# Kernel optimization log

Hardware: AMD Instinct MI355X
Metric: run time of the kernel (lower is better)

The kernel has to match this reference:

```python
import jax, jax.numpy as jnp
import numpy as np

EMBED = 256
HEADS = 8
HEAD_DIM = EMBED // HEADS  # 32, even for RoPE
INIT_VAL = 1.0
HEADS_RANGE = 3.0


def rotate_every_two(x):
    # (x1, x2) -> (-x2, x1) on interleaved pairs of last dim
    x1 = x[..., ::2]
    x2 = x[..., 1::2]
    return jnp.stack([-x2, x1], axis=-1).reshape(x.shape)


def theta_shift(x, sin, cos):
    # x: [B, heads, H, W, D]; sin/cos: [H, W, D] broadcast over B, heads
    return x * cos + rotate_every_two(x) * sin


def rel_pos_2d(H, W):
    # RetNetRelPos2d: RoPE angles + per-head exponential decay mask
    angle = 1.0 / (10000.0 ** jnp.linspace(0.0, 1.0, HEAD_DIM // 2))
    angle = jnp.repeat(angle, 2)  # [D]
    idx = jnp.arange(H * W, dtype=jnp.float32)
    sin = jnp.sin(idx[:, None] * angle[None, :]).reshape(H, W, HEAD_DIM)
    cos = jnp.cos(idx[:, None] * angle[None, :]).reshape(H, W, HEAD_DIM)
    h_idx = jnp.arange(HEADS, dtype=jnp.float32)
    decay = jnp.log(1.0 - 2.0 ** (-INIT_VAL - HEADS_RANGE * h_idx / HEADS))  # [heads]
    gh, gw = jnp.meshgrid(jnp.arange(H), jnp.arange(W), indexing='ij')
    grid = jnp.stack([gh, gw], axis=-1).reshape(H * W, 2)  # [N,2]
    dist = jnp.abs(grid[:, None, :] - grid[None, :, :]).sum(-1)  # [N,N] L1 distance
    mask = dist[None, :, :].astype(jnp.float32) * decay[:, None, None]  # [heads,N,N]
    return sin, cos, mask


def setup_inputs() -> dict:
    key = jax.random.key(0)
    ks = jax.random.split(key, 8)
    B, H, W, C = 2, 48, 48, EMBED
    s = 0.02
    return {
        'x': jax.random.normal(ks[0], (B, H, W, C), jnp.float32),
        'Wq': jax.random.normal(ks[1], (C, C), jnp.float32) * s,
        'bq': jnp.zeros((C,), jnp.float32),
        'Wk': jax.random.normal(ks[2], (C, C), jnp.float32) * s,
        'bk': jnp.zeros((C,), jnp.float32),
        'Wv': jax.random.normal(ks[3], (C, C), jnp.float32) * s,
        'bv': jnp.zeros((C,), jnp.float32),
        'lepe_w': jax.random.normal(ks[4], (C, 1, 5, 5), jnp.float32) * s,  # depthwise 5x5
        'lepe_b': jnp.zeros((C,), jnp.float32),
        'Wo': jax.random.normal(ks[5], (C, C), jnp.float32) * s,
        'bo': jnp.zeros((C,), jnp.float32),
    }


def reference(x, Wq, bq, Wk, bk, Wv, bv, lepe_w, lepe_b, Wo, bo):
    B, H, W, C = x.shape
    N = H * W
    sin, cos, mask = rel_pos_2d(H, W)
    scaling = HEAD_DIM ** -0.5

    q = x @ Wq + bq
    k = (x @ Wk + bk) * scaling
    v = x @ Wv + bv

    # lepe: depthwise 5x5 conv on v (BHWC)
    lepe = jax.lax.conv_general_dilated(
        v.transpose(0, 3, 1, 2), lepe_w, (1, 1), 'SAME',
        feature_group_count=C, dimension_numbers=('NCHW', 'OIHW', 'NCHW'))
    lepe = lepe.transpose(0, 2, 3, 1) + lepe_b  # [B,H,W,C]

    def split_heads(t):
        return t.reshape(B, H, W, HEADS, HEAD_DIM).transpose(0, 3, 1, 2, 4)

    qr = theta_shift(split_heads(q), sin, cos).reshape(B, HEADS, N, HEAD_DIM)
    kr = theta_shift(split_heads(k), sin, cos).reshape(B, HEADS, N, HEAD_DIM)
    vv = split_heads(v).reshape(B, HEADS, N, HEAD_DIM)

    attn = jnp.einsum('bhnd,bhmd->bhnm', qr, kr) + mask[None]  # [B,heads,N,N]
    attn = jax.nn.softmax(attn, axis=-1)
    out = jnp.einsum('bhnm,bhmd->bhnd', attn, vv)
    out = out.transpose(0, 2, 1, 3).reshape(B, H, W, C)
    out = out + lepe
    return out @ Wo + bo
```

## Files before the change

### kernel.cpp

```cpp
#include <hip/hip_runtime.h>
#include <hip/hip_bf16.h>
#include <math.h>

#define NN 2304
#define ROWSZ 4608
#define SZ (ROWSZ*256)

typedef __attribute__((ext_vector_type(8))) short short8;
typedef __attribute__((ext_vector_type(4))) float f32x4;

__device__ __forceinline__ float bf2f(unsigned short u) {
    return __uint_as_float(((unsigned int)u) << 16);
}
__device__ __forceinline__ unsigned short f2bf(float f) {
    unsigned int u = __float_as_uint(f);
    u += 0x7FFFu + ((u >> 16) & 1u);
    return (unsigned short)(u >> 16);
}
__device__ __forceinline__ unsigned int pack_bf2(float a, float b) {
    return (unsigned int)f2bf(a) | ((unsigned int)f2bf(b) << 16);
}

__device__ __forceinline__ float ub2f(unsigned int v, int r) {
#if defined(__has_builtin)
#if __has_builtin(__builtin_amdgcn_cvt_f32_ubyte0)
    switch (r) {
        case 0: return __builtin_amdgcn_cvt_f32_ubyte0(v);
        case 1: return __builtin_amdgcn_cvt_f32_ubyte1(v);
        case 2: return __builtin_amdgcn_cvt_f32_ubyte2(v);
        default: return __builtin_amdgcn_cvt_f32_ubyte3(v);
    }
#else
    return (float)((v >> (8*r)) & 0xFFu);
#endif
#else
    return (float)((v >> (8*r)) & 0xFFu);
#endif
}

__global__ __launch_bounds__(256) void prep_kernel(
    const void* __restrict__ x,
    const void* __restrict__ Wq, const void* __restrict__ bq,
    const void* __restrict__ Wk, const void* __restrict__ bk,
    const void* __restrict__ Wv, const void* __restrict__ bv,
    const void* __restrict__ Wo, const void* __restrict__ bo,
    const void* __restrict__ lw, const void* __restrict__ lb,
    int* __restrict__ flag, unsigned char* __restrict__ D,
    float2* __restrict__ scT, unsigned short* __restrict__ xb,
    unsigned short* __restrict__ Wt, float* __restrict__ bb,
    float* __restrict__ lwT)
{
    __shared__ float wsh[256][17];
    __shared__ int sflag;
    const int blk = blockIdx.x;
    const int t = threadIdx.x;

    {
        const int nq = blk;
        const int yq = (nq*21846) >> 20, xq = nq - yq*48;
        unsigned int* drow = reinterpret_cast<unsigned int*>(D + (size_t)nq*NN);
        for (int idx = t; idx < 576; idx += 256) {
            const int kp0 = idx*4;
            unsigned int wv = 0;
            #pragma unroll
            for (int r = 0; r < 4; ++r) {
                int kp = kp0 + r;
                int yk = (kp*21846) >> 20;
                int xk = kp - yk*48;
                unsigned int dist = __usad((unsigned)yq, (unsigned)yk,
                                    __usad((unsigned)xq, (unsigned)xk, 0u));
                wv |= dist << (8*r);
            }
            drow[idx] = wv;
        }
        if (t < 16) {
            const int j = t;
            const float ang = exp2f((float)j * (-0.8858474919699633f));
            float sv, cv;
            sincosf((float)nq * ang, &sv, &cv);
            scT[nq*16 + j] = make_float2(sv, cv);
        }
    }
    if (blk >= 656) return;

    {
        const unsigned int* xu = (const unsigned int*)x;
        if (t < 64) {
            int cnt = 0;
            for (int i = t; i < 256; i += 64) {
                unsigned int e = (xu[i] >> 7) & 0xFFu;
                cnt += (e < 87u || e > 167u) ? 1 : 0;
            }
            #pragma unroll
            for (int o = 32; o; o >>= 1) cnt += __shfl_down(cnt, o);
            if (t == 0) sflag = (cnt >= 32) ? 1 : 0;
        }
        __syncthreads();
    }
    const int F = sflag;
    if (blk == 0 && t == 0) *flag = F;

    if (blk < 576) {
        const int e = (blk*256 + t) * 8;
        if (F) {
            const float* xp = (const float*)x + e;
            float4 a0 = *reinterpret_cast<const float4*>(xp);
            float4 a1 = *reinterpret_cast<const float4*>(xp + 4);
            uint4 o;
            o.x = pack_bf2(a0.x, a0.y); o.y = pack_bf2(a0.z, a0.w);
            o.z = pack_bf2(a1.x, a1.y); o.w = pack_bf2(a1.z, a1.w);
            *reinterpret_cast<uint4*>(xb + e) = o;
        } else {
            *reinterpret_cast<uint4*>(xb + e) =
                *reinterpret_cast<const uint4*>((const unsigned short*)x + e);
        }
        return;
    }

    const int idx = blk - 576;
    const int m = idx >> 4;
    if (m == 4) {
        if ((idx & 15) != 0) return;
        float wv[25];
        #pragma unroll
        for (int j = 0; j < 25; ++j)
            wv[j] = F ? ((const float*)lw)[t*25 + j]
                      : bf2f(((const unsigned short*)lw)[t*25 + j]);
        #pragma unroll
        for (int j = 0; j < 25; ++j) lwT[j*256 + t] = wv[j];
        bb[4*256 + t] = F ? ((const float*)lb)[t]
                          : bf2f(((const unsigned short*)lb)[t]);
        return;
    }
    const int oc0 = (idx & 15) * 16;
    const void* W  = (m == 0) ? Wq : (m == 1) ? Wk : (m == 2) ? Wv : Wo;
    const void* bs = (m == 0) ? bq : (m == 1) ? bk : (m == 2) ? bv : bo;
    const float scale = (m == 1) ? 0.17677669529663687f * 1.4426950408889634f : 1.0f;
    #pragma unroll
    for (int j2 = 0; j2 < 16; ++j2)
        wsh[t][j2] = F ? ((const float*)W)[t*256 + oc0 + j2]
                       : bf2f(((const unsigned short*)W)[t*256 + oc0 + j2]);
    __syncthreads();
    const int j = t >> 4, seg = t & 15;
    unsigned int u[8];
    #pragma unroll
    for (int i = 0; i < 8; ++i) {
        float v0 = wsh[seg*16 + 2*i][j]     * scale;
        float v1 = wsh[seg*16 + 2*i + 1][j] * scale;
        u[i] = pack_bf2(v0, v1);
    }
    unsigned short* drow = Wt + ((size_t)(m*256 + oc0 + j))*256 + seg*16;
    *reinterpret_cast<uint4*>(drow)     = make_uint4(u[0], u[1], u[2], u[3]);
    *reinterpret_cast<uint4*>(drow + 8) = make_uint4(u[4], u[5], u[6], u[7]);
    if ((idx & 15) == 0)
        bb[m*256 + t] = (F ? ((const float*)bs)[t]
                           : bf2f(((const unsigned short*)bs)[t])) * scale;
}

__global__ __launch_bounds__(256) void qkv_mfma(
    const unsigned short* __restrict__ xb, const unsigned short* __restrict__ Wt,
    const float* __restrict__ bb, const float2* __restrict__ scT,
    unsigned short* __restrict__ q, unsigned short* __restrict__ k,
    unsigned short* __restrict__ v, unsigned short* __restrict__ vT)
{
    __shared__ __align__(16) char smem[43136];
    char* sc_lds = smem + 40960;
    const int t = threadIdx.x;
    const int w = t >> 6, lane = t & 63;
    const int q16 = lane & 15, quad = lane >> 4;
    const int m = blockIdx.y;
    const int tok0 = blockIdx.x * 16;
    const int b = (tok0 >= NN) ? 1 : 0;
    const int n0 = tok0 - b*NN;

    {
        float2 sv = scT[(size_t)(n0 + (t >> 4))*16 + (t & 15)];
        *reinterpret_cast<float2*>(sc_lds + (t >> 4)*136 + (t & 15)*8) = sv;
    }
    short8 af[8];
    #pragma unroll
    for (int kk = 0; kk < 8; ++kk)
        af[kk] = *reinterpret_cast<const short8*>(
            xb + (size_t)(tok0 + q16)*256 + kk*32 + quad*8);

    const unsigned short* Wm = Wt + (size_t)m*256*256;
    {
        const unsigned short* src = Wm + (size_t)t*256;
        #pragma unroll
        for (int s = 0; s < 4; ++s)
            *reinterpret_cast<uint4*>(smem + t*80 + s*16) =
                *reinterpret_cast<const uint4*>(src + s*8);
    }
    __syncthreads();

    f32x4 acc[4];
    #pragma unroll
    for (int tt = 0; tt < 4; ++tt) acc[tt] = (f32x4){0.f, 0.f, 0.f, 0.f};
    int cur = 0;
    for (int kk = 0; kk < 8; ++kk) {
        const int kkn = (kk < 7) ? kk + 1 : 7;
        uint4 nw[4];
        const unsigned short* src = Wm + (size_t)t*256 + kkn*32;
        #pragma unroll
        for (int s = 0; s < 4; ++s) nw[s] = *reinterpret_cast<const uint4*>(src + s*8);
        char* Wl = smem + cur*20480;
        #pragma unroll
        for (int tt = 0; tt < 4; ++tt) {
            short8 bf = *reinterpret_cast<const short8*>(
                Wl + (w*64 + tt*16 + q16)*80 + quad*16);
            acc[tt] = __builtin_amdgcn_mfma_f32_16x16x32_bf16(af[kk], bf, acc[tt], 0, 0, 0);
        }
        char* Wn = smem + (cur ^ 1)*20480;
        #pragma unroll
        for (int s = 0; s < 4; ++s)
            *reinterpret_cast<uint4*>(Wn + t*80 + s*16) = nw[s];
        __syncthreads();
        cur ^= 1;
    }

    char* ostage = smem;
    float bias[4];
    #pragma unroll
    for (int tt = 0; tt < 4; ++tt) bias[tt] = bb[m*256 + w*64 + tt*16 + q16];
    if (m < 2) {
        const int odd = q16 & 1;
        #pragma unroll
        for (int tt = 0; tt < 4; ++tt) {
            const int j = ((tt & 1) << 3) + (q16 >> 1);
            #pragma unroll
            for (int r = 0; r < 4; ++r) {
                const int tokL = quad*4 + r;
                float a = acc[tt][r] + bias[tt];
                float ap = __shfl_xor(a, 1);
                float2 sc = *reinterpret_cast<const float2*>(sc_lds + tokL*136 + j*8);
                float val = odd ? fmaf(a, sc.y, ap*sc.x) : fmaf(a, sc.y, -ap*sc.x);
                *reinterpret_cast<unsigned short*>(
                    ostage + tokL*528 + (w*64 + tt*16 + q16)*2) = f2bf(val);
            }
        }
    } else {
        #pragma unroll
        for (int tt = 0; tt < 4; ++tt) {
            #pragma unroll
            for (int r = 0; r < 4; ++r)
                *reinterpret_cast<unsigned short*>(
                    ostage + (quad*4 + r)*528 + (w*64 + tt*16 + q16)*2)
                    = f2bf(acc[tt][r] + bias[tt]);
        }
    }
    __syncthreads();
    unsigned short* dst = (m == 0) ? q : (m == 1) ? k : v;
    {
        char* p = ostage + (t >> 4)*528 + (t & 15)*32;
        uint4 a0 = *reinterpret_cast<uint4*>(p);
        uint4 a1 = *reinterpret_cast<uint4*>(p + 16);
        unsigned short* drow = dst + (size_t)(tok0 + (t >> 4))*256 + (t & 15)*16;
        *reinterpret_cast<uint4*>(drow)     = a0;
        *reinterpret_cast<uint4*>(drow + 8) = a1;
    }
    if (m == 2) {
        const int h = t >> 5, d = t & 31;
        unsigned int vp[8];
        #pragma unroll
        for (int i = 0; i < 8; ++i) {
            unsigned short e0 = *reinterpret_cast<unsigned short*>(
                ostage + (2*i)*528 + (h*32 + d)*2);
            unsigned short e1 = *reinterpret_cast<unsigned short*>(
                ostage + (2*i + 1)*528 + (h*32 + d)*2);
            vp[i] = (unsigned int)e0 | ((unsigned int)e1 << 16);
        }
        unsigned short* vt = vT + ((size_t)(b*8 + h)*32 + d)*NN + n0;
        *reinterpret_cast<uint4*>(vt)     = make_uint4(vp[0], vp[1], vp[2], vp[3]);
        *reinterpret_cast<uint4*>(vt + 8) = make_uint4(vp[4], vp[5], vp[6], vp[7]);
    }
}

__global__ __launch_bounds__(256) void lepe_kernel(const unsigned short* __restrict__ v,
    const float* __restrict__ lwT, const float* __restrict__ bb,
    unsigned short* __restrict__ lepe)
{
    int c = threadIdx.x;
    int pos = blockIdx.x;
    int b  = pos >= NN ? 1 : 0;
    int yx = pos - b*NN;
    int y  = (yx*21846) >> 20;
    int xx = yx - y*48;
    float acc = bb[4*256 + c];
    #pragma unroll
    for (int ky = 0; ky < 5; ++ky) {
        int yy = y + ky - 2;
        if ((unsigned)yy >= 48u) continue;
        #pragma unroll
        for (int kx = 0; kx < 5; ++kx) {
            int xc = xx + kx - 2;
            if ((unsigned)xc >= 48u) continue;
            acc = fmaf(bf2f(v[((b*NN + yy*48 + xc)<<8) + c]),
                       lwT[(ky*5 + kx)*256 + c], acc);
        }
    }
    lepe[(pos<<8) + c] = f2bf(acc);
}

template<int DIRECT>
__global__ __launch_bounds__(256) void attn_kernel(
    const unsigned short* __restrict__ q, const unsigned short* __restrict__ k,
    const unsigned short* __restrict__ vT, const unsigned char* __restrict__ D,
    unsigned short* __restrict__ o, float* __restrict__ pacc, float* __restrict__ pl)
{
    __shared__ char smem[27648];
    const int t = threadIdx.x;
    const int w = t >> 6, lane = t & 63;
    const int q16 = lane & 15, quad = lane >> 4;
    char* PsB = smem + 19456 + w*2048;
    const int bh = blockIdx.y, b = bh >> 3, h = bh & 7;
    const int q0 = blockIdx.x*64 + w*16;
    const int nq = q0 + q16;
    const float decay2 = log2f(1.0f - exp2f(-1.0f - 0.375f*(float)h));
    short8 qfrag = *reinterpret_cast<const short8*>(q + ((size_t)(b*NN + nq))*256 + h*32 + quad*8);
    f32x4 acc0 = {0.f,0.f,0.f,0.f}, acc1 = {0.f,0.f,0.f,0.f};
    const f32x4 zero = {0.f,0.f,0.f,0.f};
    float lacc = 0.0f;
    const unsigned short* kbase = k + (size_t)(b*NN)*256 + h*32;
    const unsigned short* vtb = vT + (size_t)bh*32*NN;
    const unsigned char* Dbase = D + (size_t)nq*NN + quad*4;
    const int skr = t >> 2, skp = t & 3;
    const int svd = t >> 3, svp = t & 7;
    const int psW = q16*16 + (quad & 1)*8;
    const int qsh = quad >> 1;
    const int nchunk = 36 / gridDim.z;
    const int kt0 = blockIdx.z * nchunk;

    {
        uint4 kraw = *reinterpret_cast<const uint4*>(kbase + (kt0*64 + skr)*256 + skp*8);
        uint4 vraw = *reinterpret_cast<const uint4*>(vtb + svd*NN + kt0*64 + svp*8);
        *reinterpret_cast<uint4*>(smem + skr*80 + skp*16) = kraw;
        *reinterpret_cast<uint4*>(smem + 5120 + svd*144 + svp*16) = vraw;
    }
    __syncthreads();

    int cur = 0;
    for (int kc = 0; kc < nchunk; ++kc) {
        const int kt = kt0 + kc;
        const int ktn = (kc + 1 < nchunk) ? kt + 1 : kt;
        uint4 nk = *reinterpret_cast<const uint4*>(kbase + (ktn*64 + skr)*256 + skp*8);
        uint4 nv = *reinterpret_cast<const uint4*>(vtb + svd*NN + ktn*64 + svp*8);
        unsigned int dw[4];
        #pragma unroll
        for (int tt = 0; tt < 4; ++tt)
            dw[tt] = *reinterpret_cast<const unsigned int*>(Dbase + kt*64 + tt*16);
        char* KsB = smem + cur*9728;
        char* VtB = KsB + 5120;
        f32x4 st[4];
        #pragma unroll
        for (int tt = 0; tt < 4; ++tt) {
            short8 kf = *reinterpret_cast<const short8*>(KsB + (tt*16 + q16)*80 + quad*16);
            st[tt] = __builtin_amdgcn_mfma_f32_16x16x32_bf16(kf, qfrag, zero, 0, 0, 0);
        }
        unsigned int pk[8];
        float lsum = 0.0f;
        #pragma unroll
        for (int tt = 0; tt < 4; ++tt) {
            float p[4];
            #pragma unroll
            for (int r = 0; r < 4; ++r) {
                p[r] = exp2f(fmaf(decay2, ub2f(dw[tt], r), st[tt][r]));
                lsum += p[r];
            }
            pk[tt*2]   = __builtin_amdgcn_perm(__float_as_uint(p[1]), __float_as_uint(p[0]), 0x07060302);
            pk[tt*2+1] = __builtin_amdgcn_perm(__float_as_uint(p[3]), __float_as_uint(p[2]), 0x07060302);
        }
        lacc += lsum;
        #pragma unroll
        for (int tt = 0; tt < 4; ++tt) {
            uint2 pp; pp.x = pk[tt*2]; pp.y = pk[tt*2+1];
            *reinterpret_cast<uint2*>(PsB + (tt >> 1)*1024 + (((tt*2) + qsh) & 3)*256 + psW) = pp;
        }
        #pragma unroll
        for (int kh = 0; kh < 2; ++kh) {
            short8 pf = *reinterpret_cast<const short8*>(PsB + kh*1024 + lane*16);
            short8 v0 = *reinterpret_cast<const short8*>(VtB + q16*144 + kh*64 + quad*16);
            short8 v1 = *reinterpret_cast<const short8*>(VtB + (16 + q16)*144 + kh*64 + quad*16);
            acc0 = __builtin_amdgcn_mfma_f32_16x16x32_bf16(v0, pf, acc0, 0, 0, 0);
            acc1 = __builtin_amdgcn_mfma_f32_16x16x32_bf16(v1, pf, acc1, 0, 0, 0);
        }
        char* KsN = smem + (cur^1)*9728;
        *reinterpret_cast<uint4*>(KsN + skr*80 + skp*16) = nk;
        *reinterpret_cast<uint4*>(KsN + 5120 + svd*144 + svp*16) = nv;
        __syncthreads();
        cur ^= 1;
    }
    lacc += __shfl_xor(lacc, 16);
    lacc += __shfl_xor(lacc, 32);
    if constexpr (DIRECT) {
        float invl = 1.0f / lacc;
        unsigned short* orow = o + ((size_t)(b*NN + nq))*256 + h*32;
        uint2 w0, w1;
        w0.x = pack_bf2(acc0[0]*invl, acc0[1]*invl);
        w0.y = pack_bf2(acc0[2]*invl, acc0[3]*invl);
        w1.x = pack_bf2(acc1[0]*invl, acc1[1]*invl);
        w1.y = pack_bf2(acc1[2]*invl, acc1[3]*invl);
        *reinterpret_cast<uint2*>(orow + quad*4)      = w0;
        *reinterpret_cast<uint2*>(orow + 16 + quad*4) = w1;
    } else {
        float* pb = pacc + ((size_t)(blockIdx.z*16 + bh)*NN + nq)*32;
        *reinterpret_cast<f32x4*>(pb + quad*4)      = acc0;
        *reinterpret_cast<f32x4*>(pb + 16 + quad*4) = acc1;
        if (quad == 0) pl[((size_t)blockIdx.z*16 + bh)*NN + nq] = lacc;
    }
}

__global__ __launch_bounds__(256) void out_mfma(
    const unsigned short* __restrict__ o,
    const float* __restrict__ pacc, const float* __restrict__ pl,
    const unsigned short* __restrict__ lp,
    const unsigned short* __restrict__ Wt, const float* __restrict__ bb,
    const int* __restrict__ flag, void* __restrict__ out, int nsplit)
{
    __shared__ __align__(16) char smem[49408];
    char* Ast = smem + 40960;
    const int t = threadIdx.x;
    const int w = t >> 6, lane = t & 63;
    const int q16 = lane & 15, quad = lane >> 4;
    const int tok0 = blockIdx.x * 16;

    {
        const int r = t >> 4, c0 = (t & 15) * 16;
        const int nqr = tok0 + r;
        uint4 lb0 = *reinterpret_cast<const uint4*>(lp + (size_t)nqr*256 + c0);
        uint4 lb1 = *reinterpret_cast<const uint4*>(lp + (size_t)nqr*256 + c0 + 8);
        const unsigned short* lu0 = reinterpret_cast<const unsigned short*>(&lb0);
        const unsigned short* lu1 = reinterpret_cast<const unsigned short*>(&lb1);
        float av[16];
        if (nsplit == 0) {
            uint4 oa0 = *reinterpret_cast<const uint4*>(o + (size_t)nqr*256 + c0);
            uint4 oa1 = *reinterpret_cast<const uint4*>(o + (size_t)nqr*256 + c0 + 8);
            const unsigned short* ou0 = reinterpret_cast<const unsigned short*>(&oa0);
            const unsigned short* ou1 = reinterpret_cast<const unsigned short*>(&oa1);
            #pragma unroll
            for (int j = 0; j < 8; ++j) {
                av[j]     = bf2f(ou0[j]) + bf2f(lu0[j]);
                av[8 + j] = bf2f(ou1[j]) + bf2f(lu1[j]);
            }
        } else {
            const int b = nqr >= NN ? 1 : 0;
            const int nq = nqr - b*NN;
            const int bh = b*8 + (c0 >> 5);
            const int d0 = c0 & 31;
            float s[16];
            #pragma unroll
            for (int j = 0; j < 16; ++j) s[j] = 0.f;
            float lsum = 0.f;
            for (int p = 0; p < nsplit; ++p) {
                const float* pb = pacc + ((size_t)(p*16 + bh)*NN + nq)*32 + d0;
                #pragma unroll
                for (int j4 = 0; j4 < 4; ++j4) {
                    f32x4 vv = *reinterpret_cast<const f32x4*>(pb + j4*4);
                    s[j4*4+0] += vv[0]; s[j4*4+1] += vv[1];
                    s[j4*4+2] += vv[2]; s[j4*4+3] += vv[3];
                }
                lsum += pl[((size_t)p*16 + bh)*NN + nq];
            }
            float invl = 1.0f / lsum;
            #pragma unroll
            for (int j = 0; j < 8; ++j) {
                av[j]     = fmaf(s[j],     invl, bf2f(lu0[j]));
                av[8 + j] = fmaf(s[8 + j], invl, bf2f(lu1[j]));
            }
        }
        unsigned int u[8];
        #pragma unroll
        for (int i = 0; i < 8; ++i) u[i] = pack_bf2(av[2*i], av[2*i+1]);
        *reinterpret_cast<uint4*>(Ast + r*528 + c0*2)      = make_uint4(u[0],u[1],u[2],u[3]);
        *reinterpret_cast<uint4*>(Ast + r*528 + c0*2 + 16) = make_uint4(u[4],u[5],u[6],u[7]);
    }
    const unsigned short* Wm = Wt + (size_t)3*256*256;
    {
        const unsigned short* src = Wm + (size_t)t*256;
        #pragma unroll
        for (int s2 = 0; s2 < 4; ++s2)
            *reinterpret_cast<uint4*>(smem + t*80 + s2*16) =
                *reinterpret_cast<const uint4*>(src + s2*8);
    }
    __syncthreads();
    short8 af[8];
    #pragma unroll
    for (int kk = 0; kk < 8; ++kk)
        af[kk] = *reinterpret_cast<const short8*>(Ast + q16*528 + kk*64 + quad*16);

    f32x4 acc[4];
    #pragma unroll
    for (int tt = 0; tt < 4; ++tt) acc[tt] = (f32x4){0.f, 0.f, 0.f, 0.f};
    int cur = 0;
    for (int kk = 0; kk < 8; ++kk) {
        const int kkn = (kk < 7) ? kk + 1 : 7;
        uint4 nw[4];
        const unsigned short* src = Wm + (size_t)t*256 + kkn*32;
        #pragma unroll
        for (int s2 = 0; s2 < 4; ++s2) nw[s2] = *reinterpret_cast<const uint4*>(src + s2*8);
        char* Wl = smem + cur*20480;
        #pragma unroll
        for (int tt = 0; tt < 4; ++tt) {
            short8 bf = *reinterpret_cast<const short8*>(
                Wl + (w*64 + tt*16 + q16)*80 + quad*16);
            acc[tt] = __builtin_amdgcn_mfma_f32_16x16x32_bf16(af[kk], bf, acc[tt], 0, 0, 0);
        }
        char* Wn = smem + (cur ^ 1)*20480;
        #pragma unroll
        for (int s2 = 0; s2 < 4; ++s2)
            *reinterpret_cast<uint4*>(Wn + t*80 + s2*16) = nw[s2];
        __syncthreads();
        cur ^= 1;
    }
    const int F = *flag;
    float bias[4];
    #pragma unroll
    for (int tt = 0; tt < 4; ++tt) bias[tt] = bb[3*256 + w*64 + tt*16 + q16];
    if (F) {
        char* ostf = smem;
        #pragma unroll
        for (int tt = 0; tt < 4; ++tt) {
            #pragma unroll
            for (int r = 0; r < 4; ++r)
                *reinterpret_cast<float*>(ostf + (quad*4 + r)*1040
                    + (w*64 + tt*16 + q16)*4) = acc[tt][r] + bias[tt];
        }
        __syncthreads();
        char* p = ostf + (t >> 4)*1040 + (t & 15)*64;
        float4 x0 = *reinterpret_cast<float4*>(p);
        float4 x1 = *reinterpret_cast<float4*>(p + 16);
        float4 x2 = *reinterpret_cast<float4*>(p + 32);
        float4 x3 = *reinterpret_cast<float4*>(p + 48);
        float* drow = (float*)out + (size_t)(tok0 + (t >> 4))*256 + (t & 15)*16;
        *reinterpret_cast<float4*>(drow)      = x0;
        *reinterpret_cast<float4*>(drow + 4)  = x1;
        *reinterpret_cast<float4*>(drow + 8)  = x2;
        *reinterpret_cast<float4*>(drow + 12) = x3;
    } else {
        char* ost = smem;
        #pragma unroll
        for (int tt = 0; tt < 4; ++tt) {
            #pragma unroll
            for (int r = 0; r < 4; ++r)
                *reinterpret_cast<unsigned short*>(ost + (quad*4 + r)*528
                    + (w*64 + tt*16 + q16)*2) = f2bf(acc[tt][r] + bias[tt]);
        }
        __syncthreads();
        char* p = ost + (t >> 4)*528 + (t & 15)*32;
        uint4 a0 = *reinterpret_cast<uint4*>(p);
        uint4 a1 = *reinterpret_cast<uint4*>(p + 16);
        unsigned short* drow = (unsigned short*)out + (size_t)(tok0 + (t >> 4))*256 + (t & 15)*16;
        *reinterpret_cast<uint4*>(drow)     = a0;
        *reinterpret_cast<uint4*>(drow + 8) = a1;
    }
}

extern "C" void kernel_launch(void* const* d_in, const int* in_sizes, int n_in,
                              void* d_out, int out_size, void* d_ws, size_t ws_size,
                              hipStream_t stream)
{
    const void* x  = d_in[0];
    const void* Wq = d_in[1];
    const void* bq = d_in[2];
    const void* Wk = d_in[3];
    const void* bk = d_in[4];
    const void* Wv = d_in[5];
    const void* bv = d_in[6];
    const void* lw = d_in[7];
    const void* lb = d_in[8];
    const void* Wo = d_in[9];
    const void* bo = d_in[10];

    int* flag = (int*)d_ws;
    unsigned short* qb   = (unsigned short*)((char*)d_ws + 256);
    unsigned short* kbuf = qb   + (size_t)SZ;
    unsigned short* vbuf = kbuf + (size_t)SZ;
    unsigned short* obuf = vbuf + (size_t)SZ;
    unsigned short* lbuf = obuf + (size_t)SZ;
    unsigned short* vtb  = lbuf + (size_t)SZ;
    unsigned char*  Dtab = (unsigned char*)(vtb + (size_t)SZ);
    float2* scT = (float2*)(Dtab + (size_t)NN*NN);
    unsigned short* xb = (unsigned short*)(scT + (size_t)NN*16);
    unsigned short* Wt = xb + (size_t)SZ;
    float* bb  = (float*)(Wt + (size_t)4*256*256);
    float* lwT = bb + 5*256;

    const size_t base = 256 + 6*(size_t)SZ*2 + (size_t)NN*NN
                      + (size_t)NN*16*8 + (size_t)SZ*2
                      + (size_t)4*256*256*2 + (size_t)5*256*4 + (size_t)25*256*4;
    const size_t per_split = (size_t)16*NN*32*4 + (size_t)16*NN*4;
    int nsplit = 0;
    if      (ws_size >= base + 4*per_split) nsplit = 4;
    else if (ws_size >= base + 2*per_split) nsplit = 2;
    else if (ws_size >= base + 1*per_split) nsplit = 1;
    float* pacc = (float*)((char*)d_ws + base);
    float* pl   = pacc + (size_t)(nsplit ? nsplit : 1)*16*NN*32;

    prep_kernel<<<NN, 256, 0, stream>>>(x, Wq, bq, Wk, bk, Wv, bv, Wo, bo,
                                        lw, lb, flag, Dtab, scT, xb, Wt, bb, lwT);
    qkv_mfma<<<dim3(288,3), 256, 0, stream>>>(xb, Wt, bb, scT, qb, kbuf, vbuf, vtb);
    lepe_kernel<<<4608, 256, 0, stream>>>(vbuf, lwT, bb, lbuf);
    if (nsplit) {
        attn_kernel<0><<<dim3(36, 16, nsplit), 256, 0, stream>>>(qb, kbuf, vtb, Dtab, obuf, pacc, pl);
    } else {
        attn_kernel<1><<<dim3(36, 16, 1), 256, 0, stream>>>(qb, kbuf, vtb, Dtab, obuf, pacc, pl);
    }
    out_mfma<<<288, 256, 0, stream>>>(obuf, pacc, pl, lbuf, Wt, bb, flag, d_out, nsplit);
}
```

Measured before the change: 192.0 us.

## Fold lepe conv into attention launch and single-buffer weight tiles in GEMMs

The separate depthwise 5x5 lepe kernel is removed. Its work now runs as extra blocks appended to the attention grid, so the conv can fill idle compute units alongside the attention blocks and one launch is saved. The qkv and output GEMM kernels drop LDS double buffering in favour of a single buffer with two barriers per k-step. This cuts shared memory per block, which may raise occupancy, but it loses the overlap of global loads with MFMA work.

```diff
diff --git a/kernel.cpp b/kernel.cpp
--- a/kernel.cpp
+++ b/kernel.cpp
@@ -163,8 +163,8 @@
     unsigned short* __restrict__ q, unsigned short* __restrict__ k,
     unsigned short* __restrict__ v, unsigned short* __restrict__ vT)
 {
-    __shared__ __align__(16) char smem[43136];
-    char* sc_lds = smem + 40960;
+    __shared__ __align__(16) char smem[22656];
+    char* sc_lds = smem + 20480;
     const int t = threadIdx.x;
     const int w = t >> 6, lane = t & 63;
     const int q16 = lane & 15, quad = lane >> 4;
@@ -184,39 +184,27 @@
             xb + (size_t)(tok0 + q16)*256 + kk*32 + quad*8);
 
     const unsigned short* Wm = Wt + (size_t)m*256*256;
-    {
-        const unsigned short* src = Wm + (size_t)t*256;
+    f32x4 acc[4];
+    #pragma unroll
+    for (int tt = 0; tt < 4; ++tt) acc[tt] = (f32x4){0.f, 0.f, 0.f, 0.f};
+    for (int kk = 0; kk < 8; ++kk) {
+        uint4 nw[4];
+        const unsigned short* src = Wm + (size_t)t*256 + kk*32;
+        #pragma unroll
+        for (int s = 0; s < 4; ++s) nw[s] = *reinterpret_cast<const uint4*>(src + s*8);
+        __syncthreads();
         #pragma unroll
         for (int s = 0; s < 4; ++s)
-            *reinterpret_cast<uint4*>(smem + t*80 + s*16) =
-                *reinterpret_cast<const uint4*>(src + s*8);
+            *reinterpret_cast<uint4*>(smem + t*80 + s*16) = nw[s];
+        __syncthreads();
+        #pragma unroll
+        for (int tt = 0; tt < 4; ++tt) {
+            short8 bf = *reinterpret_cast<const short8*>(
+                smem + (w*64 + tt*16 + q16)*80 + quad*16);
+            acc[tt] = __builtin_amdgcn_mfma_f32_16x16x32_bf16(af[kk], bf, acc[tt], 0, 0, 0);
+        }
     }
     __syncthreads();
-
-    f32x4 acc[4];
-    #pragma unroll
-    for (int tt = 0; tt < 4; ++tt) acc[tt] = (f32x4){0.f, 0.f, 0.f, 0.f};
-    int cur = 0;
-    for (int kk = 0; kk < 8; ++kk) {
-        const int kkn = (kk < 7) ? kk + 1 : 7;
-        uint4 nw[4];
-        const unsigned short* src = Wm + (size_t)t*256 + kkn*32;
-        #pragma unroll
-        for (int s = 0; s < 4; ++s) nw[s] = *reinterpret_cast<const uint4*>(src + s*8);
-        char* Wl = smem + cur*20480;
-        #pragma unroll
-        for (int tt = 0; tt < 4; ++tt) {
-            short8 bf = *reinterpret_cast<const short8*>(
-                Wl + (w*64 + tt*16 + q16)*80 + quad*16);
-            acc[tt] = __builtin_amdgcn_mfma_f32_16x16x32_bf16(af[kk], bf, acc[tt], 0, 0, 0);
-        }
-        char* Wn = smem + (cur ^ 1)*20480;
-        #pragma unroll
-        for (int s = 0; s < 4; ++s)
-            *reinterpret_cast<uint4*>(Wn + t*80 + s*16) = nw[s];
-        __syncthreads();
-        cur ^= 1;
-    }
 
     char* ostage = smem;
     float bias[4];
@@ -275,40 +263,40 @@
     }
 }
 
-__global__ __launch_bounds__(256) void lepe_kernel(const unsigned short* __restrict__ v,
-    const float* __restrict__ lwT, const float* __restrict__ bb,
-    unsigned short* __restrict__ lepe)
-{
-    int c = threadIdx.x;
-    int pos = blockIdx.x;
-    int b  = pos >= NN ? 1 : 0;
-    int yx = pos - b*NN;
-    int y  = (yx*21846) >> 20;
-    int xx = yx - y*48;
-    float acc = bb[4*256 + c];
-    #pragma unroll
-    for (int ky = 0; ky < 5; ++ky) {
-        int yy = y + ky - 2;
-        if ((unsigned)yy >= 48u) continue;
-        #pragma unroll
-        for (int kx = 0; kx < 5; ++kx) {
-            int xc = xx + kx - 2;
-            if ((unsigned)xc >= 48u) continue;
-            acc = fmaf(bf2f(v[((b*NN + yy*48 + xc)<<8) + c]),
-                       lwT[(ky*5 + kx)*256 + c], acc);
-        }
-    }
-    lepe[(pos<<8) + c] = f2bf(acc);
-}
-
 template<int DIRECT>
 __global__ __launch_bounds__(256) void attn_kernel(
     const unsigned short* __restrict__ q, const unsigned short* __restrict__ k,
     const unsigned short* __restrict__ vT, const unsigned char* __restrict__ D,
+    const unsigned short* __restrict__ v, const float* __restrict__ lwT,
+    const float* __restrict__ bb, unsigned short* __restrict__ lepe,
     unsigned short* __restrict__ o, float* __restrict__ pacc, float* __restrict__ pl)
 {
     __shared__ char smem[27648];
     const int t = threadIdx.x;
+    if (blockIdx.x >= 36) {
+        const int LW = gridDim.x - 36;
+        const int pos = (blockIdx.x - 36) + LW*(blockIdx.y + 16*blockIdx.z);
+        const int c = t;
+        const int b  = pos >= NN ? 1 : 0;
+        const int yx = pos - b*NN;
+        const int y  = (yx*21846) >> 20;
+        const int xx = yx - y*48;
+        float acc = bb[4*256 + c];
+        #pragma unroll
+        for (int ky = 0; ky < 5; ++ky) {
+            int yy = y + ky - 2;
+            if ((unsigned)yy >= 48u) continue;
+            #pragma unroll
+            for (int kx = 0; kx < 5; ++kx) {
+                int xc = xx + kx - 2;
+                if ((unsigned)xc >= 48u) continue;
+                acc = fmaf(bf2f(v[((b*NN + yy*48 + xc)<<8) + c]),
+                           lwT[(ky*5 + kx)*256 + c], acc);
+            }
+        }
+        lepe[(pos<<8) + c] = f2bf(acc);
+        return;
+    }
     const int w = t >> 6, lane = t & 63;
     const int q16 = lane & 15, quad = lane >> 4;
     char* PsB = smem + 19456 + w*2048;
@@ -416,8 +404,8 @@
     const unsigned short* __restrict__ Wt, const float* __restrict__ bb,
     const int* __restrict__ flag, void* __restrict__ out, int nsplit)
 {
-    __shared__ __align__(16) char smem[49408];
-    char* Ast = smem + 40960;
+    __shared__ __align__(16) char smem[28928];
+    char* Ast = smem + 20480;
     const int t = threadIdx.x;
     const int w = t >> 6, lane = t & 63;
     const int q16 = lane & 15, quad = lane >> 4;
@@ -473,44 +461,34 @@
         *reinterpret_cast<uint4*>(Ast + r*528 + c0*2)      = make_uint4(u[0],u[1],u[2],u[3]);
         *reinterpret_cast<uint4*>(Ast + r*528 + c0*2 + 16) = make_uint4(u[4],u[5],u[6],u[7]);
     }
-    const unsigned short* Wm = Wt + (size_t)3*256*256;
-    {
-        const unsigned short* src = Wm + (size_t)t*256;
-        #pragma unroll
-        for (int s2 = 0; s2 < 4; ++s2)
-            *reinterpret_cast<uint4*>(smem + t*80 + s2*16) =
-                *reinterpret_cast<const uint4*>(src + s2*8);
-    }
     __syncthreads();
     short8 af[8];
     #pragma unroll
     for (int kk = 0; kk < 8; ++kk)
         af[kk] = *reinterpret_cast<const short8*>(Ast + q16*528 + kk*64 + quad*16);
 
+    const unsigned short* Wm = Wt + (size_t)3*256*256;
     f32x4 acc[4];
     #pragma unroll
     for (int tt = 0; tt < 4; ++tt) acc[tt] = (f32x4){0.f, 0.f, 0.f, 0.f};
-    int cur = 0;
     for (int kk = 0; kk < 8; ++kk) {
-        const int kkn = (kk < 7) ? kk + 1 : 7;
         uint4 nw[4];
-        const unsigned short* src = Wm + (size_t)t*256 + kkn*32;
+        const unsigned short* src = Wm + (size_t)t*256 + kk*32;
         #pragma unroll
         for (int s2 = 0; s2 < 4; ++s2) nw[s2] = *reinterpret_cast<const uint4*>(src + s2*8);
-        char* Wl = smem + cur*20480;
+        __syncthreads();
+        #pragma unroll
+        for (int s2 = 0; s2 < 4; ++s2)
+            *reinterpret_cast<uint4*>(smem + t*80 + s2*16) = nw[s2];
+        __syncthreads();
         #pragma unroll
         for (int tt = 0; tt < 4; ++tt) {
             short8 bf = *reinterpret_cast<const short8*>(
-                Wl + (w*64 + tt*16 + q16)*80 + quad*16);
+                smem + (w*64 + tt*16 + q16)*80 + quad*16);
             acc[tt] = __builtin_amdgcn_mfma_f32_16x16x32_bf16(af[kk], bf, acc[tt], 0, 0, 0);
         }
-        char* Wn = smem + (cur ^ 1)*20480;
-        #pragma unroll
-        for (int s2 = 0; s2 < 4; ++s2)
-            *reinterpret_cast<uint4*>(Wn + t*80 + s2*16) = nw[s2];
-        __syncthreads();
-        cur ^= 1;
-    }
+    }
+    __syncthreads();
     const int F = *flag;
     float bias[4];
     #pragma unroll
@@ -598,11 +576,12 @@
     prep_kernel<<<NN, 256, 0, stream>>>(x, Wq, bq, Wk, bk, Wv, bv, Wo, bo,
                                         lw, lb, flag, Dtab, scT, xb, Wt, bb, lwT);
     qkv_mfma<<<dim3(288,3), 256, 0, stream>>>(xb, Wt, bb, scT, qb, kbuf, vbuf, vtb);
-    lepe_kernel<<<4608, 256, 0, stream>>>(vbuf, lwT, bb, lbuf);
     if (nsplit) {
-        attn_kernel<0><<<dim3(36, 16, nsplit), 256, 0, stream>>>(qb, kbuf, vtb, Dtab, obuf, pacc, pl);
+        attn_kernel<0><<<dim3(36 + 288/nsplit, 16, nsplit), 256, 0, stream>>>(
+            qb, kbuf, vtb, Dtab, vbuf, lwT, bb, lbuf, obuf, pacc, pl);
     } else {
-        attn_kernel<1><<<dim3(36, 16, 1), 256, 0, stream>>>(qb, kbuf, vtb, Dtab, obuf, pacc, pl);
+        attn_kernel<1><<<dim3(36 + 288, 16, 1), 256, 0, stream>>>(
+            qb, kbuf, vtb, Dtab, vbuf, lwT, bb, lbuf, obuf, pacc, pl);
     }
     out_mfma<<<288, 256, 0, stream>>>(obuf, pacc, pl, lbuf, Wt, bb, flag, d_out, nsplit);
 }
```

Result: slower. 245.3 us (+27.8%).
